# Optimization experiments

Hardware: AMD Instinct MI355X
Metric: run time of the kernel (lower is better)

Reference implementation:

```python
import jax, jax.numpy as jnp
import numpy as np

EMBED_DIM = 1024
NUM_HEADS = 16
HEAD_DIM = EMBED_DIM // NUM_HEADS


def setup_inputs() -> dict:
    key = jax.random.key(0)
    k_x, k_wqkv, k_bqkv, k_wo, k_bo = jax.random.split(key, 5)
    bound = 1.0 / np.sqrt(EMBED_DIM)
    x = jax.random.normal(k_x, (2, 2048, EMBED_DIM), dtype=jnp.float32)
    # torch Linear weight is [out, in]; store as [in, out] for x @ W
    W_qkv = jax.random.uniform(k_wqkv, (EMBED_DIM, 3 * EMBED_DIM), minval=-bound, maxval=bound, dtype=jnp.float32)
    b_qkv = jax.random.uniform(k_bqkv, (3 * EMBED_DIM,), minval=-bound, maxval=bound, dtype=jnp.float32)
    W_out = jax.random.uniform(k_wo, (EMBED_DIM, EMBED_DIM), minval=-bound, maxval=bound, dtype=jnp.float32)
    b_out = jax.random.uniform(k_bo, (EMBED_DIM,), minval=-bound, maxval=bound, dtype=jnp.float32)
    return {"x": x, "W_qkv": W_qkv, "b_qkv": b_qkv, "W_out": W_out, "b_out": b_out}


def reference(x, W_qkv, b_qkv, W_out, b_out):
    B, T, D = x.shape
    H, Hd = NUM_HEADS, HEAD_DIM
    qkv = x @ W_qkv + b_qkv                      # [B,T,3D]
    qkv = qkv.reshape(B, T, 3, H, Hd)
    q = qkv[:, :, 0].transpose(0, 2, 1, 3)       # [B,H,T,Hd]
    k = qkv[:, :, 1].transpose(0, 2, 1, 3)
    v = qkv[:, :, 2].transpose(0, 2, 1, 3)
    scores = jnp.einsum('bhqd,bhkd->bhqk', q, k) / jnp.sqrt(jnp.float32(Hd))
    attn = jax.nn.softmax(scores, axis=-1)       # [B,H,T,T]
    out = jnp.einsum('bhqk,bhkd->bhqd', attn, v) # [B,H,T,Hd]
    out = out.transpose(0, 2, 1, 3).reshape(B, T, D)
    return out @ W_out + b_out
```

## Files before the change

kernel.cpp:

```cpp
#include <hip/hip_runtime.h>
#include <hip/hip_bf16.h>

#define B_   2
#define T_   2048
#define D_   1024
#define H_   16
#define HD_  64
#define M_TOT (B_*T_)
#define N_QKV (3*D_)

typedef __attribute__((ext_vector_type(8))) short bf16x8;
typedef __attribute__((ext_vector_type(4))) float f32x4;
typedef __attribute__((ext_vector_type(16))) float f32x16;

static __device__ __forceinline__ short f2bf(float f) {
    union { __hip_bfloat16 h; short s; } u;
    u.h = __float2bfloat16(f);
    return u.s;
}
static __device__ __forceinline__ unsigned pack2(float a, float b) {
    return (unsigned)(unsigned short)f2bf(a) | ((unsigned)(unsigned short)f2bf(b) << 16);
}
static __device__ __forceinline__ float exp2_fast(float x) {
    return __builtin_amdgcn_exp2f(x);
}
static __device__ __forceinline__ f32x16 zero16() {
    f32x16 z;
    #pragma unroll
    for (int i = 0; i < 16; ++i) z[i] = 0.f;
    return z;
}
static __device__ __forceinline__ void gload16(const void* g, void* l) {
    __builtin_amdgcn_global_load_lds(
        (__attribute__((address_space(1))) unsigned int*)(unsigned long long)g,
        (__attribute__((address_space(3))) unsigned int*)l, 16, 0, 0);
}

__global__ __launch_bounds__(256) void convert_x(const float* __restrict__ x,
                                                 short* __restrict__ xb, int n8) {
    int i = blockIdx.x * blockDim.x + threadIdx.x;
    if (i >= n8) return;
    const float4* p = (const float4*)x + (size_t)i * 2;
    float4 a = p[0], b = p[1];
    bf16x8 o;
    o[0]=f2bf(a.x); o[1]=f2bf(a.y); o[2]=f2bf(a.z); o[3]=f2bf(a.w);
    o[4]=f2bf(b.x); o[5]=f2bf(b.y); o[6]=f2bf(b.z); o[7]=f2bf(b.w);
    *((bf16x8*)xb + i) = o;
}

__global__ __launch_bounds__(256) void transpose_convert(const float* __restrict__ in,
                                                         short* __restrict__ out,
                                                         int K, int N) {
    __shared__ short tile[64][65];
    int k0 = blockIdx.y * 64, n0 = blockIdx.x * 64;
    int t = threadIdx.x;
    #pragma unroll
    for (int i = 0; i < 16; ++i) {
        int idx = i * 256 + t;
        int r = idx >> 6, c = idx & 63;
        tile[r][c] = f2bf(in[(size_t)(k0 + r) * N + n0 + c]);
    }
    __syncthreads();
    #pragma unroll
    for (int i = 0; i < 16; ++i) {
        int idx = i * 256 + t;
        int r = idx >> 6, c = idx & 63;
        out[(size_t)(n0 + r) * K + k0 + c] = tile[c][r];
    }
}

#define QSC 0.18033688f
template<int BM, int BN, int MODE>
__global__ __launch_bounds__(256)
void gemm_dl(const short* __restrict__ A, const short* __restrict__ BT,
             const float* __restrict__ bias, int M, int N, int K,
             short* __restrict__ qo, short* __restrict__ ko,
             short* __restrict__ vo, float* __restrict__ fo) {
    constexpr int BUF = (BM + BN) * 64;
    constexpr int NL = (BM + BN) / 64;
    __shared__ char smem[2 * BUF];
    const int t = threadIdx.x, w = t >> 6, l = t & 63;
    const int qi_l = l & 15, hi_l = l >> 4;
    const int m0 = blockIdx.y * BM, n0 = blockIdx.x * BN;
    const int wr = w >> 1, wc = w & 1;
    constexpr int MI = BM / 32, NI = BN / 32;

    f32x4 acc[MI][NI];
    #pragma unroll
    for (int mi = 0; mi < MI; ++mi)
        #pragma unroll
        for (int ni = 0; ni < NI; ++ni)
            acc[mi][ni] = (f32x4){0.f, 0.f, 0.f, 0.f};

    const int lrow = l >> 2;
    const int lch  = ((l & 3) ^ (lrow & 3)) * 8;

    auto stage = [&](char* dst, int k0) {
        #pragma unroll
        for (int i = 0; i < BM / 64; ++i) {
            int rb = w * (BM / 4) + i * 16;
            gload16(A + (size_t)(m0 + rb + lrow) * K + k0 + lch, dst + rb * 64);
        }
        #pragma unroll
        for (int i = 0; i < BN / 64; ++i) {
            int rb = w * (BN / 4) + i * 16;
            gload16(BT + (size_t)(n0 + rb + lrow) * K + k0 + lch, dst + BM * 64 + rb * 64);
        }
    };

    stage(smem, 0);
    int cur = 0;
    for (int k0 = 0; k0 < K; k0 += 32) {
        if (k0 + 32 < K) {
            stage(smem + (cur ^ 1) * BUF, k0 + 32);
            if constexpr (NL == 4)      asm volatile("s_waitcnt vmcnt(4)" ::: "memory");
            else if constexpr (NL == 3) asm volatile("s_waitcnt vmcnt(3)" ::: "memory");
            else                        asm volatile("s_waitcnt vmcnt(0)" ::: "memory");
        } else {
            asm volatile("s_waitcnt vmcnt(0)" ::: "memory");
        }
        __builtin_amdgcn_s_barrier();

        char* sA = smem + cur * BUF;
        char* sB = sA + BM * 64;
        bf16x8 af[MI], bfr[NI];
        #pragma unroll
        for (int mi = 0; mi < MI; ++mi) {
            int row = wr * (BM / 2) + mi * 16 + qi_l;
            int ad = row * 64 + ((hi_l ^ (row & 3)) * 16);
            af[mi] = *(const bf16x8*)(sA + ad);
        }
        #pragma unroll
        for (int ni = 0; ni < NI; ++ni) {
            int row = wc * (BN / 2) + ni * 16 + qi_l;
            int ad = row * 64 + ((hi_l ^ (row & 3)) * 16);
            bfr[ni] = *(const bf16x8*)(sB + ad);
        }
        #pragma unroll
        for (int mi = 0; mi < MI; ++mi)
            #pragma unroll
            for (int ni = 0; ni < NI; ++ni)
                acc[mi][ni] = __builtin_amdgcn_mfma_f32_16x16x32_bf16(af[mi], bfr[ni], acc[mi][ni], 0, 0, 0);

        __builtin_amdgcn_s_barrier();
        cur ^= 1;
    }

    #pragma unroll
    for (int mi = 0; mi < MI; ++mi) {
        int rbase = m0 + wr * (BM / 2) + mi * 16 + 4 * hi_l;
        #pragma unroll
        for (int ni = 0; ni < NI; ++ni) {
            int n = n0 + wc * (BN / 2) + ni * 16 + qi_l;
            float bv = bias[n];
            #pragma unroll
            for (int r = 0; r < 4; ++r) {
                int mm = rbase + r;
                float c = acc[mi][ni][r] + bv;
                if (MODE == 0) {
                    int which = n >> 10, rest = n & 1023;
                    int h = rest >> 6, d = rest & 63;
                    int b = mm >> 11, tq = mm & 2047;
                    size_t bh = (size_t)(b * H_ + h);
                    if (which == 0)      qo[(bh * T_ + tq) * HD_ + d] = f2bf(c * QSC);
                    else if (which == 1) ko[(bh * T_ + tq) * HD_ + d] = f2bf(c);
                    else                 vo[(bh * HD_ + d) * T_ + tq] = f2bf(c);
                } else {
                    fo[(size_t)mm * N + n] = c;
                }
            }
        }
    }
}

__global__ __launch_bounds__(512)
void attn(const short* __restrict__ q, const short* __restrict__ k,
          const short* __restrict__ vt, short* __restrict__ ao) {
    __shared__ char smem[32768];

    const int t = threadIdx.x, w = t >> 6, l = t & 63;
    const int q32 = l & 31, hi2 = l >> 5;
    const int swz = (l & 7) << 4;
    const int bh = blockIdx.y;
    const int q0 = blockIdx.x * 256 + w * 32;

    const short* qptr = q + ((size_t)bh * T_ + q0) * HD_;
    const short* kbase = k + (size_t)bh * T_ * HD_;
    const short* vbase = vt + (size_t)bh * HD_ * T_;

    const int srow = w * 8 + (l >> 3);
    const int sch  = ((l & 7) ^ (l >> 3)) * 8;

    bf16x8 qa[4];
    #pragma unroll
    for (int kc = 0; kc < 4; ++kc)
        qa[kc] = *(const bf16x8*)(qptr + q32 * HD_ + kc * 16 + hi2 * 8);

    f32x16 o0 = zero16(), o1 = zero16();
    float m = -1e30f, lsum = 0.f;

    gload16(kbase + (size_t)srow * HD_ + sch, smem + srow * 128);
    gload16(vbase + (size_t)srow * T_ + sch,  smem + 8192 + srow * 128);
    __syncthreads();

    int cur = 0;
    for (int kb = 0; kb < T_; kb += 64) {
        char* sK = smem + cur * 16384;
        char* sV = sK + 8192;
        if (kb + 64 < T_) {
            char* nK = smem + (cur ^ 1) * 16384;
            gload16(kbase + (size_t)(kb + 64 + srow) * HD_ + sch, nK + srow * 128);
            gload16(vbase + (size_t)srow * T_ + (kb + 64) + sch,  nK + 8192 + srow * 128);
        }

        f32x16 s0 = zero16(), s1 = zero16();
        #pragma unroll
        for (int kc = 0; kc < 4; ++kc) {
            int off = (kc * 32 + hi2 * 16) ^ swz;
            bf16x8 kf0 = *(const bf16x8*)(sK + q32 * 128 + off);
            s0 = __builtin_amdgcn_mfma_f32_32x32x16_bf16(kf0, qa[kc], s0, 0, 0, 0);
            bf16x8 kf1 = *(const bf16x8*)(sK + (32 + q32) * 128 + off);
            s1 = __builtin_amdgcn_mfma_f32_32x32x16_bf16(kf1, qa[kc], s1, 0, 0, 0);
        }

        float a8[8];
        #pragma unroll
        for (int i = 0; i < 8; ++i)
            a8[i] = fmaxf(fmaxf(s0[i], s0[i + 8]), fmaxf(s1[i], s1[i + 8]));
        float b4_0 = fmaxf(a8[0], a8[1]), b4_1 = fmaxf(a8[2], a8[3]);
        float b4_2 = fmaxf(a8[4], a8[5]), b4_3 = fmaxf(a8[6], a8[7]);
        float tm = fmaxf(fmaxf(b4_0, b4_1), fmaxf(b4_2, b4_3));
        tm = fmaxf(tm, __shfl_xor(tm, 32));

        if (!__all(tm <= m + 8.f)) {
            float mnew = fmaxf(m, tm);
            float fsc = exp2_fast(m - mnew);
            lsum *= fsc;
            #pragma unroll
            for (int i = 0; i < 16; ++i) { o0[i] *= fsc; o1[i] *= fsc; }
            m = mnew;
        }

        #pragma unroll
        for (int i = 0; i < 16; ++i) {
            s0[i] = exp2_fast(s0[i] - m);
            s1[i] = exp2_fast(s1[i] - m);
        }
        float p8[8];
        #pragma unroll
        for (int i = 0; i < 8; ++i)
            p8[i] = (s0[i] + s0[i + 8]) + (s1[i] + s1[i + 8]);
        float psum = ((p8[0] + p8[1]) + (p8[2] + p8[3])) + ((p8[4] + p8[5]) + (p8[6] + p8[7]));
        psum += __shfl_xor(psum, 32);
        lsum += psum;

        unsigned pk0[8], pk1[8];
        #pragma unroll
        for (int p = 0; p < 8; ++p) {
            pk0[p] = pack2(s0[2 * p], s0[2 * p + 1]);
            pk1[p] = pack2(s1[2 * p], s1[2 * p + 1]);
        }

        #pragma unroll
        for (int c = 0; c < 4; ++c) {
            unsigned w0 = (c & 2) ? pk1[(c & 1) * 4 + 0] : pk0[(c & 1) * 4 + 0];
            unsigned w1 = (c & 2) ? pk1[(c & 1) * 4 + 1] : pk0[(c & 1) * 4 + 1];
            unsigned w2 = (c & 2) ? pk1[(c & 1) * 4 + 2] : pk0[(c & 1) * 4 + 2];
            unsigned w3 = (c & 2) ? pk1[(c & 1) * 4 + 3] : pk0[(c & 1) * 4 + 3];
            unsigned t0 = hi2 ? w0 : w2;
            unsigned t1 = hi2 ? w1 : w3;
            unsigned r0 = __shfl_xor(t0, 32);
            unsigned r1 = __shfl_xor(t1, 32);
            union { unsigned u[4]; bf16x8 v; } uf;
            uf.u[0] = hi2 ? r0 : w0;
            uf.u[1] = hi2 ? r1 : w1;
            uf.u[2] = hi2 ? w2 : r0;
            uf.u[3] = hi2 ? w3 : r1;
            bf16x8 pf = uf.v;

            int off = (c * 32 + hi2 * 16) ^ swz;
            bf16x8 vf0 = *(const bf16x8*)(sV + q32 * 128 + off);
            o0 = __builtin_amdgcn_mfma_f32_32x32x16_bf16(vf0, pf, o0, 0, 0, 0);
            bf16x8 vf1 = *(const bf16x8*)(sV + (32 + q32) * 128 + off);
            o1 = __builtin_amdgcn_mfma_f32_32x32x16_bf16(vf1, pf, o1, 0, 0, 0);
        }

        __syncthreads();
        cur ^= 1;
    }

    const float inv = 1.f / lsum;
    const int b = bh >> 4, h = bh & 15;
    const int tq = q0 + q32;
    unsigned* aou = (unsigned*)(ao + ((size_t)(b * T_ + tq)) * D_ + h * HD_);
    #pragma unroll
    for (int pr = 0; pr < 8; ++pr) {
        int d0 = 2 * (pr & 1) + 8 * (pr >> 1) + 4 * hi2;
        aou[d0 >> 1]        = pack2(o0[2 * pr] * inv, o0[2 * pr + 1] * inv);
        aou[(32 + d0) >> 1] = pack2(o1[2 * pr] * inv, o1[2 * pr + 1] * inv);
    }
}

extern "C" void kernel_launch(void* const* d_in, const int* in_sizes, int n_in,
                              void* d_out, int out_size, void* d_ws, size_t ws_size,
                              hipStream_t stream) {
    const float* x    = (const float*)d_in[0];
    const float* Wqkv = (const float*)d_in[1];
    const float* bqkv = (const float*)d_in[2];
    const float* Wout = (const float*)d_in[3];
    const float* bout = (const float*)d_in[4];
    float* out = (float*)d_out;

    char* ws = (char*)d_ws;
    short* xb  = (short*)(ws);
    short* WqT = (short*)(ws + ((size_t)8  << 20));
    short* WoT = (short*)(ws + ((size_t)14 << 20));
    short* qb  = (short*)(ws + ((size_t)16 << 20));
    short* kb  = (short*)(ws + ((size_t)24 << 20));
    short* vtb = (short*)(ws + ((size_t)32 << 20));
    short* aob = (short*)(ws + ((size_t)40 << 20));

    convert_x<<<(M_TOT * D_ / 8 + 255) / 256, 256, 0, stream>>>(x, xb, M_TOT * D_ / 8);
    transpose_convert<<<dim3(N_QKV / 64, D_ / 64), 256, 0, stream>>>(Wqkv, WqT, D_, N_QKV);
    transpose_convert<<<dim3(D_ / 64, D_ / 64), 256, 0, stream>>>(Wout, WoT, D_, D_);

    gemm_dl<128, 128, 0><<<dim3(N_QKV / 128, M_TOT / 128), 256, 0, stream>>>(
        xb, WqT, bqkv, M_TOT, N_QKV, D_, qb, kb, vtb, nullptr);

    attn<<<dim3(T_ / 256, B_ * H_), 512, 0, stream>>>(qb, kb, vtb, aob);

    gemm_dl<128, 64, 1><<<dim3(D_ / 64, M_TOT / 128), 256, 0, stream>>>(
        aob, WoT, bout, M_TOT, D_, D_, nullptr, nullptr, nullptr, out);
}
```

Baseline: 130.6 us.

## Software-pipeline attention: overlap next tile's QK MFMA with current softmax/PV

Restructures the attention key loop into a skewed pipeline: the QK^T scores for tile i+1 are computed before the softmax and PV of tile i, using two score register sets and a triple-buffered LDS ring for K/V. The aim is to let the MFMA unit run while the exp/max/pack work and the cross-lane shuffles of the previous tile are in flight, hiding that latency. In exchange it uses more LDS (48KB instead of 32KB) and holds extra accumulator registers, which may lower occupancy or cause spills at 512 threads.

```diff
diff --git a/kernel.cpp b/kernel.cpp
--- a/kernel.cpp
+++ b/kernel.cpp
@@ -176,7 +176,7 @@
 __global__ __launch_bounds__(512)
 void attn(const short* __restrict__ q, const short* __restrict__ k,
           const short* __restrict__ vt, short* __restrict__ ao) {
-    __shared__ char smem[32768];
+    __shared__ char smem[49152];
 
     const int t = threadIdx.x, w = t >> 6, l = t & 63;
     const int q32 = l & 31, hi2 = l >> 5;
@@ -199,30 +199,22 @@
     f32x16 o0 = zero16(), o1 = zero16();
     float m = -1e30f, lsum = 0.f;
 
-    gload16(kbase + (size_t)srow * HD_ + sch, smem + srow * 128);
-    gload16(vbase + (size_t)srow * T_ + sch,  smem + 8192 + srow * 128);
-    __syncthreads();
-
-    int cur = 0;
-    for (int kb = 0; kb < T_; kb += 64) {
-        char* sK = smem + cur * 16384;
-        char* sV = sK + 8192;
-        if (kb + 64 < T_) {
-            char* nK = smem + (cur ^ 1) * 16384;
-            gload16(kbase + (size_t)(kb + 64 + srow) * HD_ + sch, nK + srow * 128);
-            gload16(vbase + (size_t)srow * T_ + (kb + 64) + sch,  nK + 8192 + srow * 128);
-        }
-
-        f32x16 s0 = zero16(), s1 = zero16();
+    auto STAGE = [&](int kb, char* dst) {
+        gload16(kbase + (size_t)(kb + srow) * HD_ + sch, dst + srow * 128);
+        gload16(vbase + (size_t)srow * T_ + kb + sch,   dst + 8192 + srow * 128);
+    };
+    auto QK = [&](const char* sK, f32x16& d0, f32x16& d1) {
+        d0 = zero16(); d1 = zero16();
         #pragma unroll
         for (int kc = 0; kc < 4; ++kc) {
             int off = (kc * 32 + hi2 * 16) ^ swz;
             bf16x8 kf0 = *(const bf16x8*)(sK + q32 * 128 + off);
-            s0 = __builtin_amdgcn_mfma_f32_32x32x16_bf16(kf0, qa[kc], s0, 0, 0, 0);
+            d0 = __builtin_amdgcn_mfma_f32_32x32x16_bf16(kf0, qa[kc], d0, 0, 0, 0);
             bf16x8 kf1 = *(const bf16x8*)(sK + (32 + q32) * 128 + off);
-            s1 = __builtin_amdgcn_mfma_f32_32x32x16_bf16(kf1, qa[kc], s1, 0, 0, 0);
-        }
-
+            d1 = __builtin_amdgcn_mfma_f32_32x32x16_bf16(kf1, qa[kc], d1, 0, 0, 0);
+        }
+    };
+    auto FINISH = [&](f32x16& s0, f32x16& s1, const char* sV) {
         float a8[8];
         #pragma unroll
         for (int i = 0; i < 8; ++i)
@@ -260,7 +252,6 @@
             pk0[p] = pack2(s0[2 * p], s0[2 * p + 1]);
             pk1[p] = pack2(s1[2 * p], s1[2 * p + 1]);
         }
-
         #pragma unroll
         for (int c = 0; c < 4; ++c) {
             unsigned w0 = (c & 2) ? pk1[(c & 1) * 4 + 0] : pk0[(c & 1) * 4 + 0];
@@ -284,10 +275,30 @@
             bf16x8 vf1 = *(const bf16x8*)(sV + (32 + q32) * 128 + off);
             o1 = __builtin_amdgcn_mfma_f32_32x32x16_bf16(vf1, pf, o1, 0, 0, 0);
         }
-
+    };
+
+    f32x16 sA0, sA1, sB0, sB1;
+
+    STAGE(0, smem);
+    __syncthreads();
+    QK(smem, sA0, sA1);
+    STAGE(64, smem + 16384);
+    __syncthreads();
+
+    for (int it = 1; it < 32; ++it) {
+        char* cb = smem + (it % 3) * 16384;
+        char* pb = smem + ((it + 2) % 3) * 16384;
+        if (it & 1) {
+            QK(cb, sB0, sB1);
+            FINISH(sA0, sA1, pb + 8192);
+        } else {
+            QK(cb, sA0, sA1);
+            FINISH(sB0, sB1, pb + 8192);
+        }
+        if (it + 1 < 32) STAGE((it + 1) * 64, smem + ((it + 1) % 3) * 16384);
         __syncthreads();
-        cur ^= 1;
-    }
+    }
+    FINISH(sB0, sB1, smem + (31 % 3) * 16384 + 8192);
 
     const float inv = 1.f / lsum;
     const int b = bh >> 4, h = bh & 15;
```

New measurement: 148.4 us. +13.7%, slower.
